# Optimization experiments

Hardware: AMD Instinct MI355X
Metric: run time of the kernel (lower is better)

The kernel has to match this reference:

```python
import jax, jax.numpy as jnp
import numpy as np

B, N, C, H, E, K = 2, 2048, 1024, 4096, 8, 2
TAU = 1.0


def setup_inputs() -> dict:
    key = jax.random.key(0)
    ks = jax.random.split(key, 9)
    x = jax.random.normal(ks[0], (B, N, C), dtype=jnp.float32)
    T = B * N
    u = jax.random.uniform(ks[1], (T, E), minval=1e-6, maxval=1.0 - 1e-6)
    gumbel_noise = -jnp.log(-jnp.log(u))  # Gumbel(0,1) samples
    s = 0.02
    gate_w = jax.random.normal(ks[2], (C, E), dtype=jnp.float32) * s
    gate_b = jnp.zeros((E,), dtype=jnp.float32)
    w1 = jax.random.normal(ks[3], (E, C, H), dtype=jnp.float32) * s
    b1 = jnp.zeros((E, H), dtype=jnp.float32)
    w2 = jax.random.normal(ks[4], (E, H, C), dtype=jnp.float32) * s
    b2 = jnp.zeros((E, C), dtype=jnp.float32)
    return {"x": x, "gumbel_noise": gumbel_noise, "gate_w": gate_w,
            "gate_b": gate_b, "w1": w1, "b1": b1, "w2": w2, "b2": b2}


def reference(x, gumbel_noise, gate_w, gate_b, w1, b1, w2, b2):
    Bb, Nn, Cc = x.shape
    x_flat = x.reshape(-1, Cc)                                  # [T, C]
    logits = x_flat @ gate_w + gate_b                           # [T, E]
    # F.gumbel_softmax(hard=False, tau=1): softmax((logits + g)/tau)
    gates = jax.nn.softmax((logits + gumbel_noise) / TAU, axis=-1)
    mean_gates = gates.mean(axis=0)
    load_balance_loss = jnp.sum(mean_gates * jnp.log(mean_gates + 1e-8))
    topk_vals, topk_idxs = jax.lax.top_k(gates, K)              # [T, K]
    T = x_flat.shape[0]
    # scatter top-k gate weights into a dense [T, E] combine matrix
    comb = jnp.zeros((T, E), dtype=gates.dtype)
    comb = comb.at[jnp.arange(T)[:, None], topk_idxs].set(topk_vals)
    # dense per-expert MLP over all tokens, then weighted combine
    h = jnp.einsum('tc,ech->teh', x_flat, w1) + b1              # [T, E, H]
    h = jax.nn.gelu(h, approximate=False)                        # exact GELU (nn.GELU)
    y = jnp.einsum('teh,ehc->tec', h, w2) + b2                  # [T, E, C]
    out = jnp.einsum('te,tec->tc', comb, y)                     # [T, C]
    return out.reshape(Bb, Nn, Cc), load_balance_loss
```

## Files before the change

### kernel.cpp

```cpp
#include <hip/hip_runtime.h>
#include <math.h>

#define TT  4096
#define CC  1024
#define HH  4096
#define EE  8
#define TKN 8192

typedef _Float16 f16x8 __attribute__((ext_vector_type(8)));
typedef float    f32x4 __attribute__((ext_vector_type(4)));

#define GLD_LDS16(g, l)                                                        \
    __builtin_amdgcn_global_load_lds(                                          \
        (const __attribute__((address_space(1))) void*)(g),                    \
        (__attribute__((address_space(3))) void*)(l), 16, 0, 0)

__global__ __launch_bounds__(256) void gate_kernel(
    const float* __restrict__ x, const float* __restrict__ gn,
    const float* __restrict__ gw, const float* __restrict__ gb,
    int* __restrict__ topk_idx, float* __restrict__ topk_w,
    int* __restrict__ counts, float* __restrict__ gsum)
{
    int wave = threadIdx.x >> 6, lane = threadIdx.x & 63;
    int t = blockIdx.x * 4 + wave;
    const float* xrow = x + (size_t)t * CC;

    double acc[EE];
#pragma unroll
    for (int e = 0; e < EE; e++) acc[e] = 0.0;

#pragma unroll
    for (int i = 0; i < CC / 64; i++) {
        int c = i * 64 + lane;
        float xv = xrow[c];
        const float4* g4 = reinterpret_cast<const float4*>(gw + (size_t)c * EE);
        float4 g0 = g4[0], g1 = g4[1];
        double xd = (double)xv;
        acc[0] += xd * (double)g0.x; acc[1] += xd * (double)g0.y;
        acc[2] += xd * (double)g0.z; acc[3] += xd * (double)g0.w;
        acc[4] += xd * (double)g1.x; acc[5] += xd * (double)g1.y;
        acc[6] += xd * (double)g1.z; acc[7] += xd * (double)g1.w;
    }
#pragma unroll
    for (int e = 0; e < EE; e++)
#pragma unroll
        for (int off = 32; off > 0; off >>= 1)
            acc[e] += __shfl_xor(acc[e], off);

    double z[EE], m = -1e300;
#pragma unroll
    for (int e = 0; e < EE; e++) {
        z[e] = acc[e] + (double)gb[e] + (double)gn[(size_t)t * EE + e];
        m = fmax(m, z[e]);
    }
    double p[EE], s = 0.0;
#pragma unroll
    for (int e = 0; e < EE; e++) { p[e] = exp(z[e] - m); s += p[e]; }
    double inv = 1.0 / s;
    double g[EE];
#pragma unroll
    for (int e = 0; e < EE; e++) g[e] = p[e] * inv;

    int i1 = 0; double v1 = g[0];
#pragma unroll
    for (int e = 1; e < EE; e++) if (g[e] > v1) { v1 = g[e]; i1 = e; }
    int i2 = -1; double v2 = -1.0;
#pragma unroll
    for (int e = 0; e < EE; e++) if (e != i1 && g[e] > v2) { v2 = g[e]; i2 = e; }

    if (lane == 0) {
        topk_idx[t * 2 + 0] = i1; topk_w[t * 2 + 0] = (float)v1;
        topk_idx[t * 2 + 1] = i2; topk_w[t * 2 + 1] = (float)v2;
        atomicAdd(&counts[i1], 1);
        atomicAdd(&counts[i2], 1);
    }

    __shared__ float gp[4][EE];
    if (lane == 0) {
#pragma unroll
        for (int e = 0; e < EE; e++) gp[wave][e] = (float)g[e];
    }
    __syncthreads();
    if (threadIdx.x < EE) {
        float s4 = gp[0][threadIdx.x] + gp[1][threadIdx.x] +
                   gp[2][threadIdx.x] + gp[3][threadIdx.x];
        atomicAdd(&gsum[threadIdx.x], s4);
    }
}

__global__ __launch_bounds__(256) void transpose_f16_kernel(
    const float* __restrict__ src, _Float16* __restrict__ dst, int R, int Ccols)
{
    __shared__ float tile[64][65];
    int e = blockIdx.z;
    const float* s = src + (size_t)e * R * Ccols;
    _Float16* d = dst + (size_t)e * R * Ccols;
    int c0 = blockIdx.x * 64, r0 = blockIdx.y * 64;
    int tx = threadIdx.x, ty = threadIdx.y;
#pragma unroll
    for (int i = 0; i < 16; i++) {
        int r = ty + i * 4;
        tile[r][tx] = s[(size_t)(r0 + r) * Ccols + c0 + tx];
    }
    __syncthreads();
#pragma unroll
    for (int i = 0; i < 16; i++) {
        int c = ty + i * 4;
        d[(size_t)(c0 + c) * R + r0 + tx] = (_Float16)tile[tx][c];
    }
}

__global__ void scan_kernel(const int* __restrict__ counts, int* __restrict__ offsets,
                            const float* __restrict__ gsum, float* __restrict__ loss_out)
{
    if (threadIdx.x == 0) {
        int o = 0;
#pragma unroll
        for (int e = 0; e < EE; e++) { offsets[e] = o; o += counts[e]; }
        offsets[EE] = o;
        float L = 0.f;
#pragma unroll
        for (int e = 0; e < EE; e++) {
            float me = gsum[e] / (float)TT;
            L += me * logf(me + 1e-8f);
        }
        *loss_out = L;
    }
}

__global__ __launch_bounds__(256) void scatter_kernel(
    const int* __restrict__ topk_idx, const float* __restrict__ topk_w,
    const int* __restrict__ offsets, int* __restrict__ fill,
    int* __restrict__ rowtok, float* __restrict__ rweight)
{
    int t = blockIdx.x * 256 + threadIdx.x;
#pragma unroll
    for (int k = 0; k < 2; k++) {
        int e = topk_idx[t * 2 + k];
        int pos = offsets[e] + atomicAdd(&fill[e], 1);
        rowtok[pos] = t;
        rweight[pos] = topk_w[t * 2 + k];
    }
}

__global__ __launch_bounds__(256) void gather_kernel(
    const float* __restrict__ x, const int* __restrict__ rowtok,
    _Float16* __restrict__ xg)
{
    int p = blockIdx.x * 2 + (threadIdx.x >> 7);
    int c = (threadIdx.x & 127) * 8;
    int t = rowtok[p];
    const float4* s = reinterpret_cast<const float4*>(x + (size_t)t * CC + c);
    float4 v0 = s[0], v1 = s[1];
    f16x8 o;
    o[0] = (_Float16)v0.x; o[1] = (_Float16)v0.y;
    o[2] = (_Float16)v0.z; o[3] = (_Float16)v0.w;
    o[4] = (_Float16)v1.x; o[5] = (_Float16)v1.y;
    o[6] = (_Float16)v1.z; o[7] = (_Float16)v1.w;
    *reinterpret_cast<f16x8*>(xg + (size_t)p * CC + c) = o;
}

__global__ __launch_bounds__(256) void gemm1_kernel(
    const _Float16* __restrict__ xg, const _Float16* __restrict__ w1t,
    const float* __restrict__ b1, const int* __restrict__ offsets,
    _Float16* __restrict__ h)
{
    int e = blockIdx.z;
    int segs = offsets[e];
    int M = offsets[e + 1] - segs;
    int m0 = blockIdx.x * 128;
    if (m0 >= M) return;
    int n0 = blockIdx.y * 128;

    __shared__ __align__(16) _Float16 As[128][64];
    __shared__ __align__(16) _Float16 Bs[128][64];

    int tid = threadIdx.x;
    int wave = tid >> 6, lane = tid & 63;
    int wm = (wave >> 1) * 64, wn = (wave & 1) * 64;
    int lrow = lane & 15, kg = lane >> 4;

    const _Float16* wB = w1t + (size_t)e * HH * CC;

    const _Float16* ap[4]; const _Float16* bp[4];
    _Float16 *al[4], *bl[4];
#pragma unroll
    for (int j = 0; j < 4; j++) {
        int ch = (wave * 4 + j) * 64 + lane;
        int row = ch >> 3, kc = ch & 7;
        int rm = m0 + row; if (rm >= M) rm = M - 1;
        ap[j] = xg + (size_t)(segs + rm) * CC + kc * 8;
        bp[j] = wB + (size_t)(n0 + row) * CC + kc * 8;
        al[j] = &As[0][0] + ch * 8;
        bl[j] = &Bs[0][0] + ch * 8;
    }

    f32x4 acc[4][4];
#pragma unroll
    for (int i = 0; i < 4; i++)
#pragma unroll
        for (int j = 0; j < 4; j++)
#pragma unroll
            for (int r = 0; r < 4; r++) acc[i][j][r] = 0.f;

    for (int k0 = 0; k0 < CC; k0 += 64) {
#pragma unroll
        for (int j = 0; j < 4; j++) {
            GLD_LDS16(ap[j], al[j]);
            GLD_LDS16(bp[j], bl[j]);
            ap[j] += 64; bp[j] += 64;
        }
        __syncthreads();

        f16x8 aF[2][4], bF[2][4];
#pragma unroll
        for (int s = 0; s < 2; s++)
#pragma unroll
            for (int i = 0; i < 4; i++) {
                aF[s][i] = *reinterpret_cast<const f16x8*>(
                    &As[wm + i * 16 + lrow][s * 32 + kg * 8]);
                bF[s][i] = *reinterpret_cast<const f16x8*>(
                    &Bs[wn + i * 16 + lrow][s * 32 + kg * 8]);
            }
#pragma unroll
        for (int s = 0; s < 2; s++)
#pragma unroll
            for (int mi = 0; mi < 4; mi++)
#pragma unroll
                for (int ni = 0; ni < 4; ni++)
                    acc[mi][ni] = __builtin_amdgcn_mfma_f32_16x16x32_f16(
                        aF[s][mi], bF[s][ni], acc[mi][ni], 0, 0, 0);
        __syncthreads();
    }

    int rbase = (lane >> 4) * 4;
#pragma unroll
    for (int mi = 0; mi < 4; mi++) {
#pragma unroll
        for (int ni = 0; ni < 4; ni++) {
            int gcol = n0 + wn + ni * 16 + lrow;
            float bias = b1[(size_t)e * HH + gcol];
#pragma unroll
            for (int r = 0; r < 4; r++) {
                int rowl = m0 + wm + mi * 16 + rbase + r;
                if (rowl < M) {
                    float v = acc[mi][ni][r] + bias;
                    v = 0.5f * v * (1.0f + erff(v * 0.70710678118654752f));
                    h[(size_t)(segs + rowl) * HH + gcol] = (_Float16)v;
                }
            }
        }
    }
}

__global__ __launch_bounds__(256) void gemm2_kernel(
    const _Float16* __restrict__ h, const _Float16* __restrict__ w2t,
    const float* __restrict__ b2, const int* __restrict__ rowtok,
    const float* __restrict__ rweight, const int* __restrict__ offsets,
    float* __restrict__ out)
{
    int e = blockIdx.z;
    int segs = offsets[e];
    int M = offsets[e + 1] - segs;
    int m0 = blockIdx.x * 128;
    if (m0 >= M) return;
    int kz = blockIdx.y >> 3;
    int n0 = (blockIdx.y & 7) * 128;

    __shared__ __align__(16) _Float16 As[128][64];
    __shared__ __align__(16) _Float16 Bs[128][64];
    __shared__ int toks[128];
    __shared__ float wgt[128];

    int tid = threadIdx.x;
    if (tid < 128) {
        int r = m0 + tid;
        int rr = (r < M) ? r : (M - 1);
        toks[tid] = rowtok[segs + rr];
        wgt[tid] = rweight[segs + rr];
    }

    int wave = tid >> 6, lane = tid & 63;
    int wm = (wave >> 1) * 64, wn = (wave & 1) * 64;
    int lrow = lane & 15, kg = lane >> 4;

    const _Float16* wB = w2t + (size_t)e * CC * HH;
    int kbeg = kz * (HH / 2);

    const _Float16* ap[4]; const _Float16* bp[4];
    _Float16 *al[4], *bl[4];
#pragma unroll
    for (int j = 0; j < 4; j++) {
        int ch = (wave * 4 + j) * 64 + lane;
        int row = ch >> 3, kc = ch & 7;
        int rm = m0 + row; if (rm >= M) rm = M - 1;
        ap[j] = h  + (size_t)(segs + rm) * HH + kbeg + kc * 8;
        bp[j] = wB + (size_t)(n0 + row) * HH + kbeg + kc * 8;
        al[j] = &As[0][0] + ch * 8;
        bl[j] = &Bs[0][0] + ch * 8;
    }

    f32x4 acc[4][4];
#pragma unroll
    for (int i = 0; i < 4; i++)
#pragma unroll
        for (int j = 0; j < 4; j++)
#pragma unroll
            for (int r = 0; r < 4; r++) acc[i][j][r] = 0.f;

    for (int k0 = 0; k0 < HH / 2; k0 += 64) {
#pragma unroll
        for (int j = 0; j < 4; j++) {
            GLD_LDS16(ap[j], al[j]);
            GLD_LDS16(bp[j], bl[j]);
            ap[j] += 64; bp[j] += 64;
        }
        __syncthreads();

        f16x8 aF[2][4], bF[2][4];
#pragma unroll
        for (int s = 0; s < 2; s++)
#pragma unroll
            for (int i = 0; i < 4; i++) {
                aF[s][i] = *reinterpret_cast<const f16x8*>(
                    &As[wm + i * 16 + lrow][s * 32 + kg * 8]);
                bF[s][i] = *reinterpret_cast<const f16x8*>(
                    &Bs[wn + i * 16 + lrow][s * 32 + kg * 8]);
            }
#pragma unroll
        for (int s = 0; s < 2; s++)
#pragma unroll
            for (int mi = 0; mi < 4; mi++)
#pragma unroll
                for (int ni = 0; ni < 4; ni++)
                    acc[mi][ni] = __builtin_amdgcn_mfma_f32_16x16x32_f16(
                        aF[s][mi], bF[s][ni], acc[mi][ni], 0, 0, 0);
        __syncthreads();
    }

    int rbase = (lane >> 4) * 4;
#pragma unroll
    for (int mi = 0; mi < 4; mi++) {
#pragma unroll
        for (int ni = 0; ni < 4; ni++) {
            int gcol = n0 + wn + ni * 16 + lrow;
            float bias = (kz == 0) ? b2[(size_t)e * CC + gcol] : 0.f;
#pragma unroll
            for (int r = 0; r < 4; r++) {
                int rowl = m0 + wm + mi * 16 + rbase + r;
                if (rowl < M) {
                    int lr = rowl - m0;
                    float v = (acc[mi][ni][r] + bias) * wgt[lr];
                    unsafeAtomicAdd(&out[(size_t)toks[lr] * CC + gcol], v);
                }
            }
        }
    }
}

extern "C" void kernel_launch(void* const* d_in, const int* in_sizes, int n_in,
                              void* d_out, int out_size, void* d_ws, size_t ws_size,
                              hipStream_t stream)
{
    const float* x  = (const float*)d_in[0];
    const float* gn = (const float*)d_in[1];
    const float* gw = (const float*)d_in[2];
    const float* gb = (const float*)d_in[3];
    const float* w1 = (const float*)d_in[4];
    const float* b1 = (const float*)d_in[5];
    const float* w2 = (const float*)d_in[6];
    const float* b2 = (const float*)d_in[7];
    float* out = (float*)d_out;

    char* w = (char*)d_ws;
    int*   counts  = (int*)(w + 0);
    int*   fill    = (int*)(w + 32);
    int*   offsets = (int*)(w + 64);
    float* gsum    = (float*)(w + 128);
    size_t off = 256;
    int*   topk_idx = (int*)(w + off);   off += (size_t)TT * 2 * 4;
    float* topk_w   = (float*)(w + off); off += (size_t)TT * 2 * 4;
    int*   rowtok   = (int*)(w + off);   off += (size_t)TKN * 4;
    float* rweight  = (float*)(w + off); off += (size_t)TKN * 4;
    _Float16* xg  = (_Float16*)(w + off); off += (size_t)TKN * CC * 2;
    _Float16* w1t = (_Float16*)(w + off); off += (size_t)EE * HH * CC * 2;
    _Float16* w2t = (_Float16*)(w + off); off += (size_t)EE * CC * HH * 2;
    _Float16* hbuf = (_Float16*)(w + off); off += (size_t)TKN * HH * 2;

    (void)hipMemsetAsync(d_out, 0, (size_t)out_size * sizeof(float), stream);
    (void)hipMemsetAsync(d_ws, 0, 256, stream);

    gate_kernel<<<TT / 4, 256, 0, stream>>>(x, gn, gw, gb, topk_idx, topk_w,
                                            counts, gsum);
    transpose_f16_kernel<<<dim3(HH / 64, CC / 64, EE), dim3(64, 4), 0, stream>>>(
        w1, w1t, CC, HH);
    transpose_f16_kernel<<<dim3(CC / 64, HH / 64, EE), dim3(64, 4), 0, stream>>>(
        w2, w2t, HH, CC);
    scan_kernel<<<1, 64, 0, stream>>>(counts, offsets, gsum, out + (size_t)TT * CC);
    scatter_kernel<<<TT / 256, 256, 0, stream>>>(topk_idx, topk_w, offsets, fill,
                                                 rowtok, rweight);
    gather_kernel<<<TKN / 2, 256, 0, stream>>>(x, rowtok, xg);
    gemm1_kernel<<<dim3(12, HH / 128, EE), 256, 0, stream>>>(xg, w1t, b1,
                                                             offsets, hbuf);
    gemm2_kernel<<<dim3(12, 2 * (CC / 128), EE), 256, 0, stream>>>(
        hbuf, w2t, b2, rowtok, rweight, offsets, out);
}
```

Measured before the change: 908.7 us.

## Double-buffer GEMM tiles, swizzle blocks across XCDs, replace atomic combine with gather pass

```diff
diff --git a/kernel.cpp b/kernel.cpp
--- a/kernel.cpp
+++ b/kernel.cpp
@@ -96,18 +96,29 @@
     const float* s = src + (size_t)e * R * Ccols;
     _Float16* d = dst + (size_t)e * R * Ccols;
     int c0 = blockIdx.x * 64, r0 = blockIdx.y * 64;
-    int tx = threadIdx.x, ty = threadIdx.y;
-#pragma unroll
-    for (int i = 0; i < 16; i++) {
-        int r = ty + i * 4;
-        tile[r][tx] = s[(size_t)(r0 + r) * Ccols + c0 + tx];
+    int tid = threadIdx.x;
+
+    int lr = tid >> 4;
+    int lc = (tid & 15) * 4;
+#pragma unroll
+    for (int i = 0; i < 4; i++) {
+        int r = lr + i * 16;
+        float4 v = *reinterpret_cast<const float4*>(
+            s + (size_t)(r0 + r) * Ccols + c0 + lc);
+        tile[r][lc + 0] = v.x; tile[r][lc + 1] = v.y;
+        tile[r][lc + 2] = v.z; tile[r][lc + 3] = v.w;
     }
     __syncthreads();
-#pragma unroll
-    for (int i = 0; i < 16; i++) {
-        int c = ty + i * 4;
-        d[(size_t)(c0 + c) * R + r0 + tx] = (_Float16)tile[tx][c];
-    }
+
+    int oc = tid >> 2;
+    int orr = (tid & 3) * 16;
+    f16x8 o0, o1;
+#pragma unroll
+    for (int j = 0; j < 8; j++) o0[j] = (_Float16)tile[orr + j][oc];
+#pragma unroll
+    for (int j = 0; j < 8; j++) o1[j] = (_Float16)tile[orr + 8 + j][oc];
+    *reinterpret_cast<f16x8*>(d + (size_t)(c0 + oc) * R + r0 + orr)     = o0;
+    *reinterpret_cast<f16x8*>(d + (size_t)(c0 + oc) * R + r0 + orr + 8) = o1;
 }
 
 __global__ void scan_kernel(const int* __restrict__ counts, int* __restrict__ offsets,
@@ -129,9 +140,8 @@
 }
 
 __global__ __launch_bounds__(256) void scatter_kernel(
-    const int* __restrict__ topk_idx, const float* __restrict__ topk_w,
-    const int* __restrict__ offsets, int* __restrict__ fill,
-    int* __restrict__ rowtok, float* __restrict__ rweight)
+    const int* __restrict__ topk_idx, const int* __restrict__ offsets,
+    int* __restrict__ fill, int* __restrict__ rowtok, int* __restrict__ posmap)
 {
     int t = blockIdx.x * 256 + threadIdx.x;
 #pragma unroll
@@ -139,7 +149,7 @@
         int e = topk_idx[t * 2 + k];
         int pos = offsets[e] + atomicAdd(&fill[e], 1);
         rowtok[pos] = t;
-        rweight[pos] = topk_w[t * 2 + k];
+        posmap[t * 2 + k] = pos;
     }
 }
 
@@ -165,15 +175,22 @@
     const float* __restrict__ b1, const int* __restrict__ offsets,
     _Float16* __restrict__ h)
 {
-    int e = blockIdx.z;
+    int GX = gridDim.x, GY = gridDim.y;
+    int nwg = GX * GY * (int)gridDim.z;
+    int f = blockIdx.x + GX * (blockIdx.y + GY * blockIdx.z);
+    int cpx = nwg >> 3;
+    f = (f & 7) * cpx + (f >> 3);
+    int bx = f % GX; int tq = f / GX; int by = tq % GY; int bz = tq / GY;
+
+    int e = bz;
     int segs = offsets[e];
     int M = offsets[e + 1] - segs;
-    int m0 = blockIdx.x * 128;
+    int m0 = bx * 128;
     if (m0 >= M) return;
-    int n0 = blockIdx.y * 128;
-
-    __shared__ __align__(16) _Float16 As[128][64];
-    __shared__ __align__(16) _Float16 Bs[128][64];
+    int n0 = by * 128;
+
+    __shared__ __align__(16) _Float16 As[2][128][64];
+    __shared__ __align__(16) _Float16 Bs[2][128][64];
 
     int tid = threadIdx.x;
     int wave = tid >> 6, lane = tid & 63;
@@ -183,7 +200,7 @@
     const _Float16* wB = w1t + (size_t)e * HH * CC;
 
     const _Float16* ap[4]; const _Float16* bp[4];
-    _Float16 *al[4], *bl[4];
+    int lofs[4];
 #pragma unroll
     for (int j = 0; j < 4; j++) {
         int ch = (wave * 4 + j) * 64 + lane;
@@ -191,8 +208,7 @@
         int rm = m0 + row; if (rm >= M) rm = M - 1;
         ap[j] = xg + (size_t)(segs + rm) * CC + kc * 8;
         bp[j] = wB + (size_t)(n0 + row) * CC + kc * 8;
-        al[j] = &As[0][0] + ch * 8;
-        bl[j] = &Bs[0][0] + ch * 8;
+        lofs[j] = ch * 8;
     }
 
     f32x4 acc[4][4];
@@ -203,24 +219,41 @@
 #pragma unroll
             for (int r = 0; r < 4; r++) acc[i][j][r] = 0.f;
 
-    for (int k0 = 0; k0 < CC; k0 += 64) {
-#pragma unroll
-        for (int j = 0; j < 4; j++) {
-            GLD_LDS16(ap[j], al[j]);
-            GLD_LDS16(bp[j], bl[j]);
-            ap[j] += 64; bp[j] += 64;
+    _Float16* A0 = &As[0][0][0];
+    _Float16* B0 = &Bs[0][0][0];
+
+#pragma unroll
+    for (int j = 0; j < 4; j++) {
+        GLD_LDS16(ap[j], A0 + lofs[j]);
+        GLD_LDS16(bp[j], B0 + lofs[j]);
+        ap[j] += 64; bp[j] += 64;
+    }
+    __syncthreads();
+
+    int cur = 0;
+    const int NIT = CC / 64;
+    for (int it = 0; it < NIT; ++it) {
+        if (it + 1 < NIT) {
+            _Float16* ad = A0 + (cur ^ 1) * (128 * 64);
+            _Float16* bd = B0 + (cur ^ 1) * (128 * 64);
+#pragma unroll
+            for (int j = 0; j < 4; j++) {
+                GLD_LDS16(ap[j], ad + lofs[j]);
+                GLD_LDS16(bp[j], bd + lofs[j]);
+                ap[j] += 64; bp[j] += 64;
+            }
         }
-        __syncthreads();
-
+        const _Float16* Ac = A0 + cur * (128 * 64);
+        const _Float16* Bc = B0 + cur * (128 * 64);
         f16x8 aF[2][4], bF[2][4];
 #pragma unroll
         for (int s = 0; s < 2; s++)
 #pragma unroll
             for (int i = 0; i < 4; i++) {
                 aF[s][i] = *reinterpret_cast<const f16x8*>(
-                    &As[wm + i * 16 + lrow][s * 32 + kg * 8]);
+                    Ac + (wm + i * 16 + lrow) * 64 + s * 32 + kg * 8);
                 bF[s][i] = *reinterpret_cast<const f16x8*>(
-                    &Bs[wn + i * 16 + lrow][s * 32 + kg * 8]);
+                    Bc + (wn + i * 16 + lrow) * 64 + s * 32 + kg * 8);
             }
 #pragma unroll
         for (int s = 0; s < 2; s++)
@@ -231,6 +264,7 @@
                     acc[mi][ni] = __builtin_amdgcn_mfma_f32_16x16x32_f16(
                         aF[s][mi], bF[s][ni], acc[mi][ni], 0, 0, 0);
         __syncthreads();
+        cur ^= 1;
     }
 
     int rbase = (lane >> 4) * 4;
@@ -255,49 +289,43 @@
 
 __global__ __launch_bounds__(256) void gemm2_kernel(
     const _Float16* __restrict__ h, const _Float16* __restrict__ w2t,
-    const float* __restrict__ b2, const int* __restrict__ rowtok,
-    const float* __restrict__ rweight, const int* __restrict__ offsets,
-    float* __restrict__ out)
-{
-    int e = blockIdx.z;
+    const float* __restrict__ b2, const int* __restrict__ offsets,
+    float* __restrict__ y)
+{
+    int GX = gridDim.x, GY = gridDim.y;
+    int nwg = GX * GY * (int)gridDim.z;
+    int f = blockIdx.x + GX * (blockIdx.y + GY * blockIdx.z);
+    int cpx = nwg >> 3;
+    f = (f & 7) * cpx + (f >> 3);
+    int bx = f % GX; int tq = f / GX; int by = tq % GY; int bz = tq / GY;
+
+    int e = bz;
     int segs = offsets[e];
     int M = offsets[e + 1] - segs;
-    int m0 = blockIdx.x * 128;
+    int m0 = bx * 128;
     if (m0 >= M) return;
-    int kz = blockIdx.y >> 3;
-    int n0 = (blockIdx.y & 7) * 128;
-
-    __shared__ __align__(16) _Float16 As[128][64];
-    __shared__ __align__(16) _Float16 Bs[128][64];
-    __shared__ int toks[128];
-    __shared__ float wgt[128];
+    int n0 = by * 128;
+
+    __shared__ __align__(16) _Float16 As[2][128][64];
+    __shared__ __align__(16) _Float16 Bs[2][128][64];
 
     int tid = threadIdx.x;
-    if (tid < 128) {
-        int r = m0 + tid;
-        int rr = (r < M) ? r : (M - 1);
-        toks[tid] = rowtok[segs + rr];
-        wgt[tid] = rweight[segs + rr];
-    }
-
     int wave = tid >> 6, lane = tid & 63;
     int wm = (wave >> 1) * 64, wn = (wave & 1) * 64;
     int lrow = lane & 15, kg = lane >> 4;
 
     const _Float16* wB = w2t + (size_t)e * CC * HH;
-    int kbeg = kz * (HH / 2);
 
     const _Float16* ap[4]; const _Float16* bp[4];
-    _Float16 *al[4], *bl[4];
+    int lofs[4];
 #pragma unroll
     for (int j = 0; j < 4; j++) {
         int ch = (wave * 4 + j) * 64 + lane;
         int row = ch >> 3, kc = ch & 7;
         int rm = m0 + row; if (rm >= M) rm = M - 1;
-        ap[j] = h  + (size_t)(segs + rm) * HH + kbeg + kc * 8;
-        bp[j] = wB + (size_t)(n0 + row) * HH + kbeg + kc * 8;
-        al[j] = &As[0][0] + ch * 8;
-        bl[j] = &Bs[0][0] + ch * 8;
+        ap[j] = h  + (size_t)(segs + rm) * HH + kc * 8;
+        bp[j] = wB + (size_t)(n0 + row) * HH + kc * 8;
+        lofs[j] = ch * 8;
     }
 
     f32x4 acc[4][4];
@@ -308,24 +336,41 @@
 #pragma unroll
             for (int r = 0; r < 4; r++) acc[i][j][r] = 0.f;
 
-    for (int k0 = 0; k0 < HH / 2; k0 += 64) {
-#pragma unroll
-        for (int j = 0; j < 4; j++) {
-            GLD_LDS16(ap[j], al[j]);
-            GLD_LDS16(bp[j], bl[j]);
-            ap[j] += 64; bp[j] += 64;
+    _Float16* A0 = &As[0][0][0];
+    _Float16* B0 = &Bs[0][0][0];
+
+#pragma unroll
+    for (int j = 0; j < 4; j++) {
+        GLD_LDS16(ap[j], A0 + lofs[j]);
+        GLD_LDS16(bp[j], B0 + lofs[j]);
+        ap[j] += 64; bp[j] += 64;
+    }
+    __syncthreads();
+
+    int cur = 0;
+    const int NIT = HH / 64;
+    for (int it = 0; it < NIT; ++it) {
+        if (it + 1 < NIT) {
+            _Float16* ad = A0 + (cur ^ 1) * (128 * 64);
+            _Float16* bd = B0 + (cur ^ 1) * (128 * 64);
+#pragma unroll
+            for (int j = 0; j < 4; j++) {
+                GLD_LDS16(ap[j], ad + lofs[j]);
+                GLD_LDS16(bp[j], bd + lofs[j]);
+                ap[j] += 64; bp[j] += 64;
+            }
         }
-        __syncthreads();
-
+        const _Float16* Ac = A0 + cur * (128 * 64);
+        const _Float16* Bc = B0 + cur * (128 * 64);
         f16x8 aF[2][4], bF[2][4];
 #pragma unroll
         for (int s = 0; s < 2; s++)
 #pragma unroll
             for (int i = 0; i < 4; i++) {
                 aF[s][i] = *reinterpret_cast<const f16x8*>(
-                    &As[wm + i * 16 + lrow][s * 32 + kg * 8]);
+                    Ac + (wm + i * 16 + lrow) * 64 + s * 32 + kg * 8);
                 bF[s][i] = *reinterpret_cast<const f16x8*>(
-                    &Bs[wn + i * 16 + lrow][s * 32 + kg * 8]);
+                    Bc + (wn + i * 16 + lrow) * 64 + s * 32 + kg * 8);
             }
 #pragma unroll
         for (int s = 0; s < 2; s++)
@@ -336,6 +381,7 @@
                     acc[mi][ni] = __builtin_amdgcn_mfma_f32_16x16x32_f16(
                         aF[s][mi], bF[s][ni], acc[mi][ni], 0, 0, 0);
         __syncthreads();
+        cur ^= 1;
     }
 
     int rbase = (lane >> 4) * 4;
@@ -344,18 +390,35 @@
 #pragma unroll
         for (int ni = 0; ni < 4; ni++) {
             int gcol = n0 + wn + ni * 16 + lrow;
-            float bias = (kz == 0) ? b2[(size_t)e * CC + gcol] : 0.f;
+            float bias = b2[(size_t)e * CC + gcol];
 #pragma unroll
             for (int r = 0; r < 4; r++) {
                 int rowl = m0 + wm + mi * 16 + rbase + r;
-                if (rowl < M) {
-                    int lr = rowl - m0;
-                    float v = (acc[mi][ni][r] + bias) * wgt[lr];
-                    unsafeAtomicAdd(&out[(size_t)toks[lr] * CC + gcol], v);
-                }
+                if (rowl < M)
+                    y[(size_t)(segs + rowl) * CC + gcol] = acc[mi][ni][r] + bias;
             }
         }
     }
+}
+
+__global__ __launch_bounds__(256) void combine_kernel(
+    const float* __restrict__ y, const int* __restrict__ posmap,
+    const float* __restrict__ topk_w, float* __restrict__ out)
+{
+    int t = blockIdx.x * 2 + (threadIdx.x >> 7);
+    int c = (threadIdx.x & 127) * 8;
+    int p0 = posmap[t * 2 + 0], p1 = posmap[t * 2 + 1];
+    float wa = topk_w[t * 2 + 0], wb = topk_w[t * 2 + 1];
+    const float4* a = reinterpret_cast<const float4*>(y + (size_t)p0 * CC + c);
+    const float4* b = reinterpret_cast<const float4*>(y + (size_t)p1 * CC + c);
+    float4 a0 = a[0], a1 = a[1], b0 = b[0], b1 = b[1];
+    float4 r0, r1;
+    r0.x = wa * a0.x + wb * b0.x; r0.y = wa * a0.y + wb * b0.y;
+    r0.z = wa * a0.z + wb * b0.z; r0.w = wa * a0.w + wb * b0.w;
+    r1.x = wa * a1.x + wb * b1.x; r1.y = wa * a1.y + wb * b1.y;
+    r1.z = wa * a1.z + wb * b1.z; r1.w = wa * a1.w + wb * b1.w;
+    float4* o = reinterpret_cast<float4*>(out + (size_t)t * CC + c);
+    o[0] = r0; o[1] = r1;
 }
 
 extern "C" void kernel_launch(void* const* d_in, const int* in_sizes, int n_in,
@@ -381,27 +444,28 @@
     int*   topk_idx = (int*)(w + off);   off += (size_t)TT * 2 * 4;
     float* topk_w   = (float*)(w + off); off += (size_t)TT * 2 * 4;
     int*   rowtok   = (int*)(w + off);   off += (size_t)TKN * 4;
-    float* rweight  = (float*)(w + off); off += (size_t)TKN * 4;
+    int*   posmap   = (int*)(w + off);   off += (size_t)TKN * 4;
     _Float16* xg  = (_Float16*)(w + off); off += (size_t)TKN * CC * 2;
     _Float16* w1t = (_Float16*)(w + off); off += (size_t)EE * HH * CC * 2;
     _Float16* w2t = (_Float16*)(w + off); off += (size_t)EE * CC * HH * 2;
     _Float16* hbuf = (_Float16*)(w + off); off += (size_t)TKN * HH * 2;
-
-    (void)hipMemsetAsync(d_out, 0, (size_t)out_size * sizeof(float), stream);
+    float* ybuf = (float*)w1t;
+
     (void)hipMemsetAsync(d_ws, 0, 256, stream);
 
     gate_kernel<<<TT / 4, 256, 0, stream>>>(x, gn, gw, gb, topk_idx, topk_w,
                                             counts, gsum);
-    transpose_f16_kernel<<<dim3(HH / 64, CC / 64, EE), dim3(64, 4), 0, stream>>>(
+    transpose_f16_kernel<<<dim3(HH / 64, CC / 64, EE), 256, 0, stream>>>(
         w1, w1t, CC, HH);
-    transpose_f16_kernel<<<dim3(CC / 64, HH / 64, EE), dim3(64, 4), 0, stream>>>(
+    transpose_f16_kernel<<<dim3(CC / 64, HH / 64, EE), 256, 0, stream>>>(
         w2, w2t, HH, CC);
     scan_kernel<<<1, 64, 0, stream>>>(counts, offsets, gsum, out + (size_t)TT * CC);
-    scatter_kernel<<<TT / 256, 256, 0, stream>>>(topk_idx, topk_w, offsets, fill,
-                                                 rowtok, rweight);
+    scatter_kernel<<<TT / 256, 256, 0, stream>>>(topk_idx, offsets, fill,
+                                                 rowtok, posmap);
     gather_kernel<<<TKN / 2, 256, 0, stream>>>(x, rowtok, xg);
     gemm1_kernel<<<dim3(12, HH / 128, EE), 256, 0, stream>>>(xg, w1t, b1,
                                                              offsets, hbuf);
-    gemm2_kernel<<<dim3(12, 2 * (CC / 128), EE), 256, 0, stream>>>(
-        hbuf, w2t, b2, rowtok, rweight, offsets, out);
-}
+    gemm2_kernel<<<dim3(12, CC / 128, EE), 256, 0, stream>>>(
+        hbuf, w2t, b2, offsets, ybuf);
+    combine_kernel<<<TT / 2, 256, 0, stream>>>(ybuf, posmap, topk_w, out);
+}
```

After: 1.002 ms. +10.2%, slower.
